# Kernel optimization log

Hardware: AMD Instinct MI355X
Metric: run time of the kernel (lower is better)

The kernel has to match this reference:

```python
import jax, jax.numpy as jnp
import numpy as np

N_NODES = 50000
N_EDGES = 800000
D_FEAT = 64          # per-node feature dim
HIDDEN = 128         # fc1 output dim; fc1 input = 2*D_FEAT


def setup_inputs() -> dict:
    key = jax.random.key(0)
    k1, k2, k3 = jax.random.split(key, 3)
    x = jax.random.normal(k1, (N_NODES, D_FEAT), dtype=jnp.float32)
    edge_index = jax.random.randint(k2, (2, N_EDGES), 0, N_NODES, dtype=jnp.int64)
    # fc1: Linear(2*D_FEAT, HIDDEN); torch Linear weight is [out, in]
    W = jax.random.normal(k3, (HIDDEN, 2 * D_FEAT), dtype=jnp.float32) * (1.0 / np.sqrt(2 * D_FEAT))
    b = jnp.zeros((HIDDEN,), dtype=jnp.float32)
    return {"x": x, "edge_index": edge_index, "W": W, "b": b}


def reference(x, edge_index, W, b):
    # Gather source-node features along edges, sum-scatter to destinations.
    src, dst = edge_index[0], edge_index[1]
    gathered = x[src]  # [E, D_FEAT] -- dominant memory traffic
    neigh = jax.ops.segment_sum(gathered, dst, num_segments=x.shape[0])  # [N, D_FEAT]
    # Concat self features with aggregated neighbor features, then Linear+ReLU.
    h = jnp.concatenate([x, neigh], axis=-1)          # [N, 2*D_FEAT]
    out = jax.nn.relu(h @ W.T + b)                    # [N, HIDDEN]
    return out
```

## Files before the change

### kernel.cpp

```cpp
#include <hip/hip_runtime.h>

#define N_NODES 50000
#define N_EDGES 800000
#define DFEAT 64
#define HID 128
#define NBKT 782
#define NSEG 196
#define SEGW 32
#define CAP 1400
#define NSTR 66

#define XB2 1563
#define WB2 8
#define EB2 196

typedef __bf16 bf16x8 __attribute__((ext_vector_type(8)));
typedef float f32x4 __attribute__((ext_vector_type(4)));

__device__ inline unsigned short f2bf(float f) {
  unsigned u = __float_as_uint(f);
  return (unsigned short)((u + 0x7FFFu + ((u >> 16) & 1u)) >> 16);
}
__device__ inline float bf2f(unsigned short h) {
  return __uint_as_float(((unsigned)h) << 16);
}

__global__ __launch_bounds__(512) void k_prep(const float* __restrict__ x,
                                              const float* __restrict__ W,
                                              const int* __restrict__ ei,
                                              unsigned short* __restrict__ xb,
                                              unsigned short* __restrict__ Wb,
                                              unsigned int* __restrict__ coarse) {
  int bid = blockIdx.x;
  const int tid = threadIdx.x;
  if (bid < XB2) {
    int t = bid * 512 + tid;
    if (t < N_NODES * DFEAT / 4) {
      float4 v = *(const float4*)&x[t * 4];
      ushort4 o = {f2bf(v.x), f2bf(v.y), f2bf(v.z), f2bf(v.w)};
      *(ushort4*)&xb[t * 4] = o;
    }
    return;
  }
  bid -= XB2;
  if (bid < WB2) {
    int t = bid * 512 + tid;
    float4 v = *(const float4*)&W[t * 4];
    ushort4 o = {f2bf(v.x), f2bf(v.y), f2bf(v.z), f2bf(v.w)};
    *(ushort4*)&Wb[t * 4] = o;
    return;
  }
  bid -= WB2;
  __shared__ int lcnt[NBKT];
  for (int i = tid; i < NBKT; i += 512) lcnt[i] = 0;
  __syncthreads();

  int e0 = (bid * 512 + tid) * 8;
  if (e0 < N_EDGES) {
    int4 sa = *(const int4*)&ei[e0];
    int4 sb = *(const int4*)&ei[e0 + 4];
    int4 da = *(const int4*)&ei[N_EDGES + e0];
    int4 db = *(const int4*)&ei[N_EDGES + e0 + 4];
    int ss[8] = {sa.x, sa.y, sa.z, sa.w, sb.x, sb.y, sb.z, sb.w};
    int dd[8] = {da.x, da.y, da.z, da.w, db.x, db.y, db.z, db.w};
#pragma unroll
    for (int i = 0; i < 8; ++i) {
      int bkt = dd[i] >> 6;
      int rank = atomicAdd(&lcnt[bkt], 1);
      if (rank < SEGW - 1)
        coarse[(size_t)bkt * (NSEG * SEGW) + bid * SEGW + 1 + rank] =
            ((unsigned)dd[i] << 16) | (unsigned)ss[i];
    }
  }
  __syncthreads();
  for (int i = tid; i < NBKT; i += 512) {
    int c = lcnt[i];
    coarse[(size_t)i * (NSEG * SEGW) + bid * SEGW] =
        (unsigned)(c < SEGW - 1 ? c : SEGW - 1);
  }
}

__global__ __launch_bounds__(512) void k_gnn(const unsigned short* __restrict__ xb,
                                             const unsigned short* __restrict__ Wb,
                                             const unsigned int* __restrict__ coarse,
                                             const float* __restrict__ bv,
                                             float* __restrict__ out) {
  __shared__ unsigned int stg[NSEG * SEGW];
  __shared__ unsigned int sq[CAP];
  __shared__ unsigned int ns_u[32 * NSTR];
  __shared__ int lcnt[64];
  __shared__ int lbase[65];

  const int tid = threadIdx.x;
  const int b = blockIdx.x;
  const int nb = b * 64;
  const unsigned int* base = coarse + (size_t)b * (NSEG * SEGW);

  if (tid < 64) lcnt[tid] = 0;
  const int NU4 = NSEG * SEGW / 4;
  for (int i = tid; i < NU4; i += 512)
    ((uint4*)stg)[i] = ((const uint4*)base)[i];
  __syncthreads();

  for (int s = tid; s < NSEG; s += 512) {
    int cs = (int)stg[s * SEGW];
    if (cs > SEGW - 1) cs = SEGW - 1;
    for (int k = 0; k < cs; ++k) {
      unsigned e = stg[s * SEGW + 1 + k] & 0x003fffffu;
      int rel = (int)(e >> 16);
      int rank = atomicAdd(&lcnt[rel], 1);
      stg[s * SEGW + 1 + k] = e | ((unsigned)rank << 22);
    }
  }
  __syncthreads();
  if (tid < 64) {
    int v = lcnt[tid];
    int inc = v;
#pragma unroll
    for (int o = 1; o < 64; o <<= 1) {
      int u = __shfl_up(inc, o);
      if (tid >= o) inc += u;
    }
    int ex = inc - v;
    lbase[tid] = ex < CAP ? ex : CAP;
    if (tid == 63) lbase[64] = inc < CAP ? inc : CAP;
  }
  __syncthreads();
  for (int s = tid; s < NSEG; s += 512) {
    int cs = (int)stg[s * SEGW];
    if (cs > SEGW - 1) cs = SEGW - 1;
    for (int k = 0; k < cs; ++k) {
      unsigned w = stg[s * SEGW + 1 + k];
      unsigned e = w & 0x003fffffu;
      int p = lbase[e >> 16] + (int)(w >> 22);
      if (p < CAP) sq[p] = e;
    }
  }
  __syncthreads();

  const int wave = tid >> 6;
  const int lane = tid & 63;
  const int g3 = lane >> 4;
  const int c = lane & 15;
  const uint2* xu2 = (const uint2*)xb;

#pragma unroll
  for (int i2 = 0; i2 < 2; ++i2) {
    int n = (wave * 4 + g3) * 2 + i2;
    int beg = lbase[n], end = lbase[n + 1];
    float A0 = 0.f, A1 = 0.f, A2 = 0.f, A3 = 0.f;
    float B0 = 0.f, B1 = 0.f, B2 = 0.f, B3 = 0.f;
    float C0 = 0.f, C1 = 0.f, C2 = 0.f, C3 = 0.f;
    float D0 = 0.f, D1 = 0.f, D2 = 0.f, D3 = 0.f;
    int j = beg;
    for (; j + 3 < end; j += 4) {
      unsigned e0 = sq[j], e1 = sq[j + 1], e2 = sq[j + 2], e3 = sq[j + 3];
      uint2 v0 = xu2[(e0 & 0xffffu) * 16 + c];
      uint2 v1 = xu2[(e1 & 0xffffu) * 16 + c];
      uint2 v2 = xu2[(e2 & 0xffffu) * 16 + c];
      uint2 v3 = xu2[(e3 & 0xffffu) * 16 + c];
      A0 += bf2f((unsigned short)(v0.x & 0xffffu)); A1 += bf2f((unsigned short)(v0.x >> 16));
      A2 += bf2f((unsigned short)(v0.y & 0xffffu)); A3 += bf2f((unsigned short)(v0.y >> 16));
      B0 += bf2f((unsigned short)(v1.x & 0xffffu)); B1 += bf2f((unsigned short)(v1.x >> 16));
      B2 += bf2f((unsigned short)(v1.y & 0xffffu)); B3 += bf2f((unsigned short)(v1.y >> 16));
      C0 += bf2f((unsigned short)(v2.x & 0xffffu)); C1 += bf2f((unsigned short)(v2.x >> 16));
      C2 += bf2f((unsigned short)(v2.y & 0xffffu)); C3 += bf2f((unsigned short)(v2.y >> 16));
      D0 += bf2f((unsigned short)(v3.x & 0xffffu)); D1 += bf2f((unsigned short)(v3.x >> 16));
      D2 += bf2f((unsigned short)(v3.y & 0xffffu)); D3 += bf2f((unsigned short)(v3.y >> 16));
    }
    for (; j < end; ++j) {
      unsigned e = sq[j];
      uint2 v = xu2[(e & 0xffffu) * 16 + c];
      A0 += bf2f((unsigned short)(v.x & 0xffffu)); A1 += bf2f((unsigned short)(v.x >> 16));
      A2 += bf2f((unsigned short)(v.y & 0xffffu)); A3 += bf2f((unsigned short)(v.y >> 16));
    }
    A0 += B0 + C0 + D0; A1 += B1 + C1 + D1;
    A2 += B2 + C2 + D2; A3 += B3 + C3 + D3;
    ns_u[(2 * c) * NSTR + n] = (unsigned)f2bf(A0) | ((unsigned)f2bf(A1) << 16);
    ns_u[(2 * c + 1) * NSTR + n] = (unsigned)f2bf(A2) | ((unsigned)f2bf(A3) << 16);
  }
  __syncthreads();

  const int g2 = wave & 3;
  const int o = wave >> 2;
  const int l15 = lane & 15;
  const int quad = lane >> 4;
  const int node0 = nb + g2 * 16;

  int anode = node0 + l15;
  if (anode >= N_NODES) anode = N_NODES - 1;
  const unsigned short* hx = xb + (size_t)anode * DFEAT;

  bf16x8 fa0 = *(const bf16x8*)(hx + quad * 8);
  bf16x8 fa1 = *(const bf16x8*)(hx + 32 + quad * 8);
  bf16x8 fa2, fa3;
  {
    int m = g2 * 16 + l15;
    union { unsigned u[4]; bf16x8 v; } c2, c3;
#pragma unroll
    for (int i = 0; i < 4; ++i) {
      c2.u[i] = ns_u[(quad * 4 + i) * NSTR + m];
      c3.u[i] = ns_u[(16 + quad * 4 + i) * NSTR + m];
    }
    fa2 = c2.v;
    fa3 = c3.v;
  }

  f32x4 accr[4];
#pragma unroll
  for (int t = 0; t < 4; ++t) accr[t] = (f32x4){0.f, 0.f, 0.f, 0.f};

#pragma unroll
  for (int t = 0; t < 4; ++t) {
    int nt = o * 4 + t;
    const unsigned short* wr = Wb + (size_t)(nt * 16 + l15) * (2 * DFEAT) + quad * 8;
    bf16x8 b0 = *(const bf16x8*)(wr);
    bf16x8 b1 = *(const bf16x8*)(wr + 32);
    bf16x8 b2 = *(const bf16x8*)(wr + 64);
    bf16x8 b3 = *(const bf16x8*)(wr + 96);
    accr[t] = __builtin_amdgcn_mfma_f32_16x16x32_bf16(fa0, b0, accr[t], 0, 0, 0);
    accr[t] = __builtin_amdgcn_mfma_f32_16x16x32_bf16(fa1, b1, accr[t], 0, 0, 0);
    accr[t] = __builtin_amdgcn_mfma_f32_16x16x32_bf16(fa2, b2, accr[t], 0, 0, 0);
    accr[t] = __builtin_amdgcn_mfma_f32_16x16x32_bf16(fa3, b3, accr[t], 0, 0, 0);
  }

#pragma unroll
  for (int t = 0; t < 4; ++t) {
    int nt = o * 4 + t;
    float bias = bv[nt * 16 + l15];
#pragma unroll
    for (int r = 0; r < 4; ++r) {
      int node = node0 + quad * 4 + r;
      if (node < N_NODES) {
        float v = accr[t][r] + bias;
        out[(size_t)node * HID + nt * 16 + l15] = v > 0.f ? v : 0.f;
      }
    }
  }
}

extern "C" void kernel_launch(void* const* d_in, const int* in_sizes, int n_in,
                              void* d_out, int out_size, void* d_ws, size_t ws_size,
                              hipStream_t stream) {
  const float* x = (const float*)d_in[0];
  const int* ei = (const int*)d_in[1];
  const float* W = (const float*)d_in[2];
  const float* b = (const float*)d_in[3];
  float* out = (float*)d_out;

  char* ws = (char*)d_ws;
  unsigned int* coarse = (unsigned int*)ws;   ws += (size_t)NBKT * NSEG * SEGW * 4;
  unsigned short* xb   = (unsigned short*)ws; ws += (size_t)N_NODES * DFEAT * 2;
  unsigned short* Wb   = (unsigned short*)ws; ws += (size_t)HID * 2 * DFEAT * 2;

  k_prep<<<XB2 + WB2 + EB2, 512, 0, stream>>>(x, W, ei, xb, Wb, coarse);
  k_gnn<<<NBKT, 512, 0, stream>>>(xb, Wb, coarse, b, out);
}
```

Baseline: 128.2 us.

## Split fused GNN into separate convert, bin, gather and FC kernels

Splits the two-kernel pipeline into four: bf16 conversion, edge binning, neighbor gather/aggregation writing bf16 sums to global memory, and an MFMA linear layer reading them back. It also pads the shared staging buffer row stride to 33 words to cut LDS bank conflicts. The split lowers per-kernel LDS use and register pressure, which may raise occupancy. The cost is two more launches and a round trip of the aggregated features through global memory.

```diff
diff --git a/kernel.cpp b/kernel.cpp
--- a/kernel.cpp
+++ b/kernel.cpp
@@ -7,8 +7,8 @@
 #define NBKT 782
 #define NSEG 196
 #define SEGW 32
+#define SSTR 33
 #define CAP 1400
-#define NSTR 66
 
 #define XB2 1563
 #define WB2 8
@@ -25,12 +25,10 @@
   return __uint_as_float(((unsigned)h) << 16);
 }
 
-__global__ __launch_bounds__(512) void k_prep(const float* __restrict__ x,
-                                              const float* __restrict__ W,
-                                              const int* __restrict__ ei,
-                                              unsigned short* __restrict__ xb,
-                                              unsigned short* __restrict__ Wb,
-                                              unsigned int* __restrict__ coarse) {
+__global__ __launch_bounds__(512) void k_cvt(const float* __restrict__ x,
+                                             const float* __restrict__ W,
+                                             unsigned short* __restrict__ xb,
+                                             unsigned short* __restrict__ Wb) {
   int bid = blockIdx.x;
   const int tid = threadIdx.x;
   if (bid < XB2) {
@@ -43,14 +41,16 @@
     return;
   }
   bid -= XB2;
-  if (bid < WB2) {
-    int t = bid * 512 + tid;
-    float4 v = *(const float4*)&W[t * 4];
-    ushort4 o = {f2bf(v.x), f2bf(v.y), f2bf(v.z), f2bf(v.w)};
-    *(ushort4*)&Wb[t * 4] = o;
-    return;
-  }
-  bid -= WB2;
+  int t = bid * 512 + tid;
+  float4 v = *(const float4*)&W[t * 4];
+  ushort4 o = {f2bf(v.x), f2bf(v.y), f2bf(v.z), f2bf(v.w)};
+  *(ushort4*)&Wb[t * 4] = o;
+}
+
+__global__ __launch_bounds__(512) void k_bin(const int* __restrict__ ei,
+                                             unsigned int* __restrict__ coarse) {
+  const int bid = blockIdx.x;
+  const int tid = threadIdx.x;
   __shared__ int lcnt[NBKT];
   for (int i = tid; i < NBKT; i += 512) lcnt[i] = 0;
   __syncthreads();
@@ -80,14 +80,12 @@
   }
 }
 
-__global__ __launch_bounds__(512) void k_gnn(const unsigned short* __restrict__ xb,
-                                             const unsigned short* __restrict__ Wb,
-                                             const unsigned int* __restrict__ coarse,
-                                             const float* __restrict__ bv,
-                                             float* __restrict__ out) {
-  __shared__ unsigned int stg[NSEG * SEGW];
+__global__ __launch_bounds__(512) void k_gather(const unsigned short* __restrict__ xb,
+                                                const unsigned int* __restrict__ coarse,
+                                                const float* __restrict__ bv,
+                                                unsigned short* __restrict__ nsg) {
+  __shared__ unsigned int stg[NSEG * SSTR];
   __shared__ unsigned int sq[CAP];
-  __shared__ unsigned int ns_u[32 * NSTR];
   __shared__ int lcnt[64];
   __shared__ int lbase[65];
 
@@ -98,18 +96,21 @@
 
   if (tid < 64) lcnt[tid] = 0;
   const int NU4 = NSEG * SEGW / 4;
-  for (int i = tid; i < NU4; i += 512)
-    ((uint4*)stg)[i] = ((const uint4*)base)[i];
+  for (int i = tid; i < NU4; i += 512) {
+    uint4 v = ((const uint4*)base)[i];
+    int s = i >> 3, w = (i & 7) * 4;
+    unsigned* p = &stg[s * SSTR + w];
+    p[0] = v.x; p[1] = v.y; p[2] = v.z; p[3] = v.w;
+  }
   __syncthreads();
 
   for (int s = tid; s < NSEG; s += 512) {
-    int cs = (int)stg[s * SEGW];
+    int cs = (int)stg[s * SSTR];
     if (cs > SEGW - 1) cs = SEGW - 1;
     for (int k = 0; k < cs; ++k) {
-      unsigned e = stg[s * SEGW + 1 + k] & 0x003fffffu;
-      int rel = (int)(e >> 16);
-      int rank = atomicAdd(&lcnt[rel], 1);
-      stg[s * SEGW + 1 + k] = e | ((unsigned)rank << 22);
+      unsigned e = stg[s * SSTR + 1 + k] & 0x003fffffu;
+      int rank = atomicAdd(&lcnt[e >> 16], 1);
+      stg[s * SSTR + 1 + k] = e | ((unsigned)rank << 22);
     }
   }
   __syncthreads();
@@ -127,10 +128,10 @@
   }
   __syncthreads();
   for (int s = tid; s < NSEG; s += 512) {
-    int cs = (int)stg[s * SEGW];
+    int cs = (int)stg[s * SSTR];
     if (cs > SEGW - 1) cs = SEGW - 1;
     for (int k = 0; k < cs; ++k) {
-      unsigned w = stg[s * SEGW + 1 + k];
+      unsigned w = stg[s * SSTR + 1 + k];
       unsigned e = w & 0x003fffffu;
       int p = lbase[e >> 16] + (int)(w >> 22);
       if (p < CAP) sq[p] = e;
@@ -176,11 +177,25 @@
     }
     A0 += B0 + C0 + D0; A1 += B1 + C1 + D1;
     A2 += B2 + C2 + D2; A3 += B3 + C3 + D3;
-    ns_u[(2 * c) * NSTR + n] = (unsigned)f2bf(A0) | ((unsigned)f2bf(A1) << 16);
-    ns_u[(2 * c + 1) * NSTR + n] = (unsigned)f2bf(A2) | ((unsigned)f2bf(A3) << 16);
-  }
-  __syncthreads();
-
+    int gn = nb + n;
+    if (gn < N_NODES) {
+      ushort4 o = {f2bf(A0), f2bf(A1), f2bf(A2), f2bf(A3)};
+      *(ushort4*)&nsg[(size_t)gn * DFEAT + 4 * c] = o;
+    }
+  }
+}
+
+__global__ __launch_bounds__(512) void k_fc(const unsigned short* __restrict__ xb,
+                                            const unsigned short* __restrict__ nsg,
+                                            const unsigned short* __restrict__ Wb,
+                                            const float* __restrict__ bv,
+                                            float* __restrict__ out) {
+  const int tid = threadIdx.x;
+  const int b = blockIdx.x;
+  const int nb = b * 64;
+
+  const int wave = tid >> 6;
+  const int lane = tid & 63;
   const int g2 = wave & 3;
   const int o = wave >> 2;
   const int l15 = lane & 15;
@@ -190,21 +205,12 @@
   int anode = node0 + l15;
   if (anode >= N_NODES) anode = N_NODES - 1;
   const unsigned short* hx = xb + (size_t)anode * DFEAT;
+  const unsigned short* hn = nsg + (size_t)anode * DFEAT;
 
   bf16x8 fa0 = *(const bf16x8*)(hx + quad * 8);
   bf16x8 fa1 = *(const bf16x8*)(hx + 32 + quad * 8);
-  bf16x8 fa2, fa3;
-  {
-    int m = g2 * 16 + l15;
-    union { unsigned u[4]; bf16x8 v; } c2, c3;
-#pragma unroll
-    for (int i = 0; i < 4; ++i) {
-      c2.u[i] = ns_u[(quad * 4 + i) * NSTR + m];
-      c3.u[i] = ns_u[(16 + quad * 4 + i) * NSTR + m];
-    }
-    fa2 = c2.v;
-    fa3 = c3.v;
-  }
+  bf16x8 fa2 = *(const bf16x8*)(hn + quad * 8);
+  bf16x8 fa3 = *(const bf16x8*)(hn + 32 + quad * 8);
 
   f32x4 accr[4];
 #pragma unroll
@@ -252,7 +258,10 @@
   unsigned int* coarse = (unsigned int*)ws;   ws += (size_t)NBKT * NSEG * SEGW * 4;
   unsigned short* xb   = (unsigned short*)ws; ws += (size_t)N_NODES * DFEAT * 2;
   unsigned short* Wb   = (unsigned short*)ws; ws += (size_t)HID * 2 * DFEAT * 2;
-
-  k_prep<<<XB2 + WB2 + EB2, 512, 0, stream>>>(x, W, ei, xb, Wb, coarse);
-  k_gnn<<<NBKT, 512, 0, stream>>>(xb, Wb, coarse, b, out);
-}
+  unsigned short* nsg  = (unsigned short*)ws; ws += (size_t)N_NODES * DFEAT * 2;
+
+  k_cvt<<<XB2 + WB2, 512, 0, stream>>>(x, W, xb, Wb);
+  k_bin<<<EB2, 512, 0, stream>>>(ei, coarse);
+  k_gather<<<NBKT, 512, 0, stream>>>(xb, coarse, b, nsg);
+  k_fc<<<NBKT, 512, 0, stream>>>(xb, nsg, Wb, b, out);
+}
```

Measured after the change: 129.7 us. Within noise of the previous version (+1.2%).

## Split bf16 features into two half tables and gather halves sequentially

Applied to the files above, without the earlier changes.

Stores the bf16 copy of x as two separate arrays holding features 0-31 and 32-63. The neighbor gather now runs in two passes, one node per 8 lanes. Each pass touches a 3.2MB table, which is meant to improve L2 hit rates for random row gathers. The staging buffer in LDS is also padded to a stride of 33 to avoid bank conflicts in the per-segment scans. In exchange, edge indices are read twice, each random access fetches only 64 bytes, and an extra barrier is added.

```diff
diff --git a/kernel.cpp b/kernel.cpp
--- a/kernel.cpp
+++ b/kernel.cpp
@@ -7,6 +7,7 @@
 #define NBKT 782
 #define NSEG 196
 #define SEGW 32
+#define SSTR 33
 #define CAP 1400
 #define NSTR 66
 
@@ -28,7 +29,8 @@
 __global__ __launch_bounds__(512) void k_prep(const float* __restrict__ x,
                                               const float* __restrict__ W,
                                               const int* __restrict__ ei,
-                                              unsigned short* __restrict__ xb,
+                                              unsigned short* __restrict__ xlo,
+                                              unsigned short* __restrict__ xhi,
                                               unsigned short* __restrict__ Wb,
                                               unsigned int* __restrict__ coarse) {
   int bid = blockIdx.x;
@@ -38,7 +40,11 @@
     if (t < N_NODES * DFEAT / 4) {
       float4 v = *(const float4*)&x[t * 4];
       ushort4 o = {f2bf(v.x), f2bf(v.y), f2bf(v.z), f2bf(v.w)};
-      *(ushort4*)&xb[t * 4] = o;
+      int node = t >> 4;
+      int f4 = (t & 15) * 4;
+      unsigned short* dst = (f4 < 32) ? &xlo[(size_t)node * 32 + f4]
+                                      : &xhi[(size_t)node * 32 + (f4 - 32)];
+      *(ushort4*)dst = o;
     }
     return;
   }
@@ -80,12 +86,49 @@
   }
 }
 
-__global__ __launch_bounds__(512) void k_gnn(const unsigned short* __restrict__ xb,
+__device__ inline void gather_half(const uint2* __restrict__ xu2,
+                                   const unsigned int* __restrict__ sq,
+                                   unsigned int* __restrict__ ns_u,
+                                   int beg, int end, int c, int n, int pb) {
+  float A0 = 0.f, A1 = 0.f, A2 = 0.f, A3 = 0.f;
+  float B0 = 0.f, B1 = 0.f, B2 = 0.f, B3 = 0.f;
+  float C0 = 0.f, C1 = 0.f, C2 = 0.f, C3 = 0.f;
+  float D0 = 0.f, D1 = 0.f, D2 = 0.f, D3 = 0.f;
+  int j = beg;
+  for (; j + 3 < end; j += 4) {
+    unsigned e0 = sq[j], e1 = sq[j + 1], e2 = sq[j + 2], e3 = sq[j + 3];
+    uint2 v0 = xu2[(e0 & 0xffffu) * 8 + c];
+    uint2 v1 = xu2[(e1 & 0xffffu) * 8 + c];
+    uint2 v2 = xu2[(e2 & 0xffffu) * 8 + c];
+    uint2 v3 = xu2[(e3 & 0xffffu) * 8 + c];
+    A0 += bf2f((unsigned short)(v0.x & 0xffffu)); A1 += bf2f((unsigned short)(v0.x >> 16));
+    A2 += bf2f((unsigned short)(v0.y & 0xffffu)); A3 += bf2f((unsigned short)(v0.y >> 16));
+    B0 += bf2f((unsigned short)(v1.x & 0xffffu)); B1 += bf2f((unsigned short)(v1.x >> 16));
+    B2 += bf2f((unsigned short)(v1.y & 0xffffu)); B3 += bf2f((unsigned short)(v1.y >> 16));
+    C0 += bf2f((unsigned short)(v2.x & 0xffffu)); C1 += bf2f((unsigned short)(v2.x >> 16));
+    C2 += bf2f((unsigned short)(v2.y & 0xffffu)); C3 += bf2f((unsigned short)(v2.y >> 16));
+    D0 += bf2f((unsigned short)(v3.x & 0xffffu)); D1 += bf2f((unsigned short)(v3.x >> 16));
+    D2 += bf2f((unsigned short)(v3.y & 0xffffu)); D3 += bf2f((unsigned short)(v3.y >> 16));
+  }
+  for (; j < end; ++j) {
+    unsigned e = sq[j];
+    uint2 v = xu2[(e & 0xffffu) * 8 + c];
+    A0 += bf2f((unsigned short)(v.x & 0xffffu)); A1 += bf2f((unsigned short)(v.x >> 16));
+    A2 += bf2f((unsigned short)(v.y & 0xffffu)); A3 += bf2f((unsigned short)(v.y >> 16));
+  }
+  A0 += B0 + C0 + D0; A1 += B1 + C1 + D1;
+  A2 += B2 + C2 + D2; A3 += B3 + C3 + D3;
+  ns_u[(pb + 2 * c) * NSTR + n]     = (unsigned)f2bf(A0) | ((unsigned)f2bf(A1) << 16);
+  ns_u[(pb + 2 * c + 1) * NSTR + n] = (unsigned)f2bf(A2) | ((unsigned)f2bf(A3) << 16);
+}
+
+__global__ __launch_bounds__(512) void k_gnn(const unsigned short* __restrict__ xlo,
+                                             const unsigned short* __restrict__ xhi,
                                              const unsigned short* __restrict__ Wb,
                                              const unsigned int* __restrict__ coarse,
                                              const float* __restrict__ bv,
                                              float* __restrict__ out) {
-  __shared__ unsigned int stg[NSEG * SEGW];
+  __shared__ unsigned int stg[NSEG * SSTR];
   __shared__ unsigned int sq[CAP];
   __shared__ unsigned int ns_u[32 * NSTR];
   __shared__ int lcnt[64];
@@ -98,18 +141,21 @@
 
   if (tid < 64) lcnt[tid] = 0;
   const int NU4 = NSEG * SEGW / 4;
-  for (int i = tid; i < NU4; i += 512)
-    ((uint4*)stg)[i] = ((const uint4*)base)[i];
+  for (int i = tid; i < NU4; i += 512) {
+    uint4 v = ((const uint4*)base)[i];
+    int s = i >> 3, w = (i & 7) * 4;
+    unsigned* p = &stg[s * SSTR + w];
+    p[0] = v.x; p[1] = v.y; p[2] = v.z; p[3] = v.w;
+  }
   __syncthreads();
 
   for (int s = tid; s < NSEG; s += 512) {
-    int cs = (int)stg[s * SEGW];
+    int cs = (int)stg[s * SSTR];
     if (cs > SEGW - 1) cs = SEGW - 1;
     for (int k = 0; k < cs; ++k) {
-      unsigned e = stg[s * SEGW + 1 + k] & 0x003fffffu;
-      int rel = (int)(e >> 16);
-      int rank = atomicAdd(&lcnt[rel], 1);
-      stg[s * SEGW + 1 + k] = e | ((unsigned)rank << 22);
+      unsigned e = stg[s * SSTR + 1 + k] & 0x003fffffu;
+      int rank = atomicAdd(&lcnt[e >> 16], 1);
+      stg[s * SSTR + 1 + k] = e | ((unsigned)rank << 22);
     }
   }
   __syncthreads();
@@ -127,10 +173,10 @@
   }
   __syncthreads();
   for (int s = tid; s < NSEG; s += 512) {
-    int cs = (int)stg[s * SEGW];
+    int cs = (int)stg[s * SSTR];
     if (cs > SEGW - 1) cs = SEGW - 1;
     for (int k = 0; k < cs; ++k) {
-      unsigned w = stg[s * SEGW + 1 + k];
+      unsigned w = stg[s * SSTR + 1 + k];
       unsigned e = w & 0x003fffffu;
       int p = lbase[e >> 16] + (int)(w >> 22);
       if (p < CAP) sq[p] = e;
@@ -140,45 +186,14 @@
 
   const int wave = tid >> 6;
   const int lane = tid & 63;
-  const int g3 = lane >> 4;
-  const int c = lane & 15;
-  const uint2* xu2 = (const uint2*)xb;
-
-#pragma unroll
-  for (int i2 = 0; i2 < 2; ++i2) {
-    int n = (wave * 4 + g3) * 2 + i2;
-    int beg = lbase[n], end = lbase[n + 1];
-    float A0 = 0.f, A1 = 0.f, A2 = 0.f, A3 = 0.f;
-    float B0 = 0.f, B1 = 0.f, B2 = 0.f, B3 = 0.f;
-    float C0 = 0.f, C1 = 0.f, C2 = 0.f, C3 = 0.f;
-    float D0 = 0.f, D1 = 0.f, D2 = 0.f, D3 = 0.f;
-    int j = beg;
-    for (; j + 3 < end; j += 4) {
-      unsigned e0 = sq[j], e1 = sq[j + 1], e2 = sq[j + 2], e3 = sq[j + 3];
-      uint2 v0 = xu2[(e0 & 0xffffu) * 16 + c];
-      uint2 v1 = xu2[(e1 & 0xffffu) * 16 + c];
-      uint2 v2 = xu2[(e2 & 0xffffu) * 16 + c];
-      uint2 v3 = xu2[(e3 & 0xffffu) * 16 + c];
-      A0 += bf2f((unsigned short)(v0.x & 0xffffu)); A1 += bf2f((unsigned short)(v0.x >> 16));
-      A2 += bf2f((unsigned short)(v0.y & 0xffffu)); A3 += bf2f((unsigned short)(v0.y >> 16));
-      B0 += bf2f((unsigned short)(v1.x & 0xffffu)); B1 += bf2f((unsigned short)(v1.x >> 16));
-      B2 += bf2f((unsigned short)(v1.y & 0xffffu)); B3 += bf2f((unsigned short)(v1.y >> 16));
-      C0 += bf2f((unsigned short)(v2.x & 0xffffu)); C1 += bf2f((unsigned short)(v2.x >> 16));
-      C2 += bf2f((unsigned short)(v2.y & 0xffffu)); C3 += bf2f((unsigned short)(v2.y >> 16));
-      D0 += bf2f((unsigned short)(v3.x & 0xffffu)); D1 += bf2f((unsigned short)(v3.x >> 16));
-      D2 += bf2f((unsigned short)(v3.y & 0xffffu)); D3 += bf2f((unsigned short)(v3.y >> 16));
-    }
-    for (; j < end; ++j) {
-      unsigned e = sq[j];
-      uint2 v = xu2[(e & 0xffffu) * 16 + c];
-      A0 += bf2f((unsigned short)(v.x & 0xffffu)); A1 += bf2f((unsigned short)(v.x >> 16));
-      A2 += bf2f((unsigned short)(v.y & 0xffffu)); A3 += bf2f((unsigned short)(v.y >> 16));
-    }
-    A0 += B0 + C0 + D0; A1 += B1 + C1 + D1;
-    A2 += B2 + C2 + D2; A3 += B3 + C3 + D3;
-    ns_u[(2 * c) * NSTR + n] = (unsigned)f2bf(A0) | ((unsigned)f2bf(A1) << 16);
-    ns_u[(2 * c + 1) * NSTR + n] = (unsigned)f2bf(A2) | ((unsigned)f2bf(A3) << 16);
-  }
+  const int g3 = lane >> 3;
+  const int c = lane & 7;
+  const int n = wave * 8 + g3;
+  const int beg = lbase[n], end = lbase[n + 1];
+
+  gather_half((const uint2*)xlo, sq, ns_u, beg, end, c, n, 0);
+  __syncthreads();
+  gather_half((const uint2*)xhi, sq, ns_u, beg, end, c, n, 16);
   __syncthreads();
 
   const int g2 = wave & 3;
@@ -189,10 +204,8 @@
 
   int anode = node0 + l15;
   if (anode >= N_NODES) anode = N_NODES - 1;
-  const unsigned short* hx = xb + (size_t)anode * DFEAT;
-
-  bf16x8 fa0 = *(const bf16x8*)(hx + quad * 8);
-  bf16x8 fa1 = *(const bf16x8*)(hx + 32 + quad * 8);
+  bf16x8 fa0 = *(const bf16x8*)(xlo + (size_t)anode * 32 + quad * 8);
+  bf16x8 fa1 = *(const bf16x8*)(xhi + (size_t)anode * 32 + quad * 8);
   bf16x8 fa2, fa3;
   {
     int m = g2 * 16 + l15;
@@ -250,9 +263,10 @@
 
   char* ws = (char*)d_ws;
   unsigned int* coarse = (unsigned int*)ws;   ws += (size_t)NBKT * NSEG * SEGW * 4;
-  unsigned short* xb   = (unsigned short*)ws; ws += (size_t)N_NODES * DFEAT * 2;
+  unsigned short* xlo  = (unsigned short*)ws; ws += (size_t)N_NODES * 32 * 2;
+  unsigned short* xhi  = (unsigned short*)ws; ws += (size_t)N_NODES * 32 * 2;
   unsigned short* Wb   = (unsigned short*)ws; ws += (size_t)HID * 2 * DFEAT * 2;
 
-  k_prep<<<XB2 + WB2 + EB2, 512, 0, stream>>>(x, W, ei, xb, Wb, coarse);
-  k_gnn<<<NBKT, 512, 0, stream>>>(xb, Wb, coarse, b, out);
-}
+  k_prep<<<XB2 + WB2 + EB2, 512, 0, stream>>>(x, W, ei, xlo, xhi, Wb, coarse);
+  k_gnn<<<NBKT, 512, 0, stream>>>(xlo, xhi, Wb, coarse, b, out);
+}
```

Result: no change. 125.9 us (-1.8%).

## Fuse prep and GNN kernels into one cooperative persistent kernel with grid sync

Applied to the files above, without the earlier changes.

Merges the binning/conversion kernel and the gather+MFMA kernel into a single cooperative launch, separated by a grid-wide barrier. Conversion blocks become grid-stride and bucket processing becomes a persistent loop over the grid. The staging buffer gets a padded stride and flattened per-edge loops instead of per-segment serial loops, and the gather unroll grows from 4 to 8 edges. This aims to remove the second launch gap and the serial per-segment work, at the cost of grid-sync overhead and fewer resident blocks per bucket pass.

```diff
diff --git a/kernel.cpp b/kernel.cpp
--- a/kernel.cpp
+++ b/kernel.cpp
@@ -1,4 +1,7 @@
 #include <hip/hip_runtime.h>
+#include <hip/hip_cooperative_groups.h>
+
+namespace cg = cooperative_groups;
 
 #define N_NODES 50000
 #define N_EDGES 800000
@@ -7,12 +10,12 @@
 #define NBKT 782
 #define NSEG 196
 #define SEGW 32
+#define SSTR 33
 #define CAP 1400
 #define NSTR 66
-
-#define XB2 1563
-#define WB2 8
-#define EB2 196
+#define GMAX 768
+#define X4 (N_NODES * DFEAT / 4)
+#define TOT4 (X4 + HID * 2 * DFEAT / 4)
 
 typedef __bf16 bf16x8 __attribute__((ext_vector_type(8)));
 typedef float f32x4 __attribute__((ext_vector_type(4)));
@@ -25,217 +28,229 @@
   return __uint_as_float(((unsigned)h) << 16);
 }
 
-__global__ __launch_bounds__(512) void k_prep(const float* __restrict__ x,
-                                              const float* __restrict__ W,
-                                              const int* __restrict__ ei,
-                                              unsigned short* __restrict__ xb,
-                                              unsigned short* __restrict__ Wb,
-                                              unsigned int* __restrict__ coarse) {
-  int bid = blockIdx.x;
-  const int tid = threadIdx.x;
-  if (bid < XB2) {
-    int t = bid * 512 + tid;
-    if (t < N_NODES * DFEAT / 4) {
-      float4 v = *(const float4*)&x[t * 4];
-      ushort4 o = {f2bf(v.x), f2bf(v.y), f2bf(v.z), f2bf(v.w)};
-      *(ushort4*)&xb[t * 4] = o;
-    }
-    return;
-  }
-  bid -= XB2;
-  if (bid < WB2) {
-    int t = bid * 512 + tid;
-    float4 v = *(const float4*)&W[t * 4];
-    ushort4 o = {f2bf(v.x), f2bf(v.y), f2bf(v.z), f2bf(v.w)};
-    *(ushort4*)&Wb[t * 4] = o;
-    return;
-  }
-  bid -= WB2;
-  __shared__ int lcnt[NBKT];
-  for (int i = tid; i < NBKT; i += 512) lcnt[i] = 0;
-  __syncthreads();
-
-  int e0 = (bid * 512 + tid) * 8;
-  if (e0 < N_EDGES) {
-    int4 sa = *(const int4*)&ei[e0];
-    int4 sb = *(const int4*)&ei[e0 + 4];
-    int4 da = *(const int4*)&ei[N_EDGES + e0];
-    int4 db = *(const int4*)&ei[N_EDGES + e0 + 4];
-    int ss[8] = {sa.x, sa.y, sa.z, sa.w, sb.x, sb.y, sb.z, sb.w};
-    int dd[8] = {da.x, da.y, da.z, da.w, db.x, db.y, db.z, db.w};
-#pragma unroll
-    for (int i = 0; i < 8; ++i) {
-      int bkt = dd[i] >> 6;
-      int rank = atomicAdd(&lcnt[bkt], 1);
-      if (rank < SEGW - 1)
-        coarse[(size_t)bkt * (NSEG * SEGW) + bid * SEGW + 1 + rank] =
-            ((unsigned)dd[i] << 16) | (unsigned)ss[i];
-    }
-  }
-  __syncthreads();
-  for (int i = tid; i < NBKT; i += 512) {
-    int c = lcnt[i];
-    coarse[(size_t)i * (NSEG * SEGW) + bid * SEGW] =
-        (unsigned)(c < SEGW - 1 ? c : SEGW - 1);
-  }
-}
-
-__global__ __launch_bounds__(512) void k_gnn(const unsigned short* __restrict__ xb,
-                                             const unsigned short* __restrict__ Wb,
-                                             const unsigned int* __restrict__ coarse,
-                                             const float* __restrict__ bv,
-                                             float* __restrict__ out) {
-  __shared__ unsigned int stg[NSEG * SEGW];
+__global__ __launch_bounds__(512, 4) void k_all(const float* __restrict__ x,
+                                                const float* __restrict__ W,
+                                                const int* __restrict__ ei,
+                                                unsigned short* __restrict__ xb,
+                                                unsigned short* __restrict__ Wb,
+                                                unsigned int* __restrict__ coarse,
+                                                const float* __restrict__ bv,
+                                                float* __restrict__ out) {
+  __shared__ unsigned int stg[NSEG * SSTR];
   __shared__ unsigned int sq[CAP];
   __shared__ unsigned int ns_u[32 * NSTR];
   __shared__ int lcnt[64];
   __shared__ int lbase[65];
 
   const int tid = threadIdx.x;
-  const int b = blockIdx.x;
-  const int nb = b * 64;
-  const unsigned int* base = coarse + (size_t)b * (NSEG * SEGW);
-
-  if (tid < 64) lcnt[tid] = 0;
-  const int NU4 = NSEG * SEGW / 4;
-  for (int i = tid; i < NU4; i += 512)
-    ((uint4*)stg)[i] = ((const uint4*)base)[i];
-  __syncthreads();
-
-  for (int s = tid; s < NSEG; s += 512) {
-    int cs = (int)stg[s * SEGW];
-    if (cs > SEGW - 1) cs = SEGW - 1;
-    for (int k = 0; k < cs; ++k) {
-      unsigned e = stg[s * SEGW + 1 + k] & 0x003fffffu;
-      int rel = (int)(e >> 16);
-      int rank = atomicAdd(&lcnt[rel], 1);
-      stg[s * SEGW + 1 + k] = e | ((unsigned)rank << 22);
+  const int bid = blockIdx.x;
+  const int grid = gridDim.x;
+
+  if (bid < NSEG) {
+    int* h = (int*)stg;
+    for (int i = tid; i < NBKT; i += 512) h[i] = 0;
+    __syncthreads();
+    int e0 = (bid * 512 + tid) * 8;
+    if (e0 < N_EDGES) {
+      int4 sa = *(const int4*)&ei[e0];
+      int4 sb = *(const int4*)&ei[e0 + 4];
+      int4 da = *(const int4*)&ei[N_EDGES + e0];
+      int4 db = *(const int4*)&ei[N_EDGES + e0 + 4];
+      int ss[8] = {sa.x, sa.y, sa.z, sa.w, sb.x, sb.y, sb.z, sb.w};
+      int dd[8] = {da.x, da.y, da.z, da.w, db.x, db.y, db.z, db.w};
+#pragma unroll
+      for (int i = 0; i < 8; ++i) {
+        int bkt = dd[i] >> 6;
+        int rank = atomicAdd(&h[bkt], 1);
+        if (rank < SEGW - 1)
+          coarse[(size_t)bkt * (NSEG * SEGW) + bid * SEGW + 1 + rank] =
+              ((unsigned)dd[i] << 16) | (unsigned)ss[i];
+      }
+    }
+    __syncthreads();
+    for (int i = tid; i < NBKT; i += 512) {
+      int c = h[i];
+      coarse[(size_t)i * (NSEG * SEGW) + bid * SEGW] =
+          (unsigned)(c < SEGW - 1 ? c : SEGW - 1);
+    }
+  } else {
+    const int ncvt = grid - NSEG;
+    for (int t = (bid - NSEG) * 512 + tid; t < TOT4; t += ncvt * 512) {
+      if (t < X4) {
+        float4 v = ((const float4*)x)[t];
+        ushort4 o = {f2bf(v.x), f2bf(v.y), f2bf(v.z), f2bf(v.w)};
+        ((ushort4*)xb)[t] = o;
+      } else {
+        float4 v = ((const float4*)W)[t - X4];
+        ushort4 o = {f2bf(v.x), f2bf(v.y), f2bf(v.z), f2bf(v.w)};
+        ((ushort4*)Wb)[t - X4] = o;
+      }
     }
   }
-  __syncthreads();
-  if (tid < 64) {
-    int v = lcnt[tid];
-    int inc = v;
-#pragma unroll
-    for (int o = 1; o < 64; o <<= 1) {
-      int u = __shfl_up(inc, o);
-      if (tid >= o) inc += u;
-    }
-    int ex = inc - v;
-    lbase[tid] = ex < CAP ? ex : CAP;
-    if (tid == 63) lbase[64] = inc < CAP ? inc : CAP;
-  }
-  __syncthreads();
-  for (int s = tid; s < NSEG; s += 512) {
-    int cs = (int)stg[s * SEGW];
-    if (cs > SEGW - 1) cs = SEGW - 1;
-    for (int k = 0; k < cs; ++k) {
-      unsigned w = stg[s * SEGW + 1 + k];
-      unsigned e = w & 0x003fffffu;
-      int p = lbase[e >> 16] + (int)(w >> 22);
-      if (p < CAP) sq[p] = e;
-    }
-  }
-  __syncthreads();
-
-  const int wave = tid >> 6;
-  const int lane = tid & 63;
-  const int g3 = lane >> 4;
-  const int c = lane & 15;
-  const uint2* xu2 = (const uint2*)xb;
-
-#pragma unroll
-  for (int i2 = 0; i2 < 2; ++i2) {
-    int n = (wave * 4 + g3) * 2 + i2;
-    int beg = lbase[n], end = lbase[n + 1];
-    float A0 = 0.f, A1 = 0.f, A2 = 0.f, A3 = 0.f;
-    float B0 = 0.f, B1 = 0.f, B2 = 0.f, B3 = 0.f;
-    float C0 = 0.f, C1 = 0.f, C2 = 0.f, C3 = 0.f;
-    float D0 = 0.f, D1 = 0.f, D2 = 0.f, D3 = 0.f;
-    int j = beg;
-    for (; j + 3 < end; j += 4) {
-      unsigned e0 = sq[j], e1 = sq[j + 1], e2 = sq[j + 2], e3 = sq[j + 3];
-      uint2 v0 = xu2[(e0 & 0xffffu) * 16 + c];
-      uint2 v1 = xu2[(e1 & 0xffffu) * 16 + c];
-      uint2 v2 = xu2[(e2 & 0xffffu) * 16 + c];
-      uint2 v3 = xu2[(e3 & 0xffffu) * 16 + c];
-      A0 += bf2f((unsigned short)(v0.x & 0xffffu)); A1 += bf2f((unsigned short)(v0.x >> 16));
-      A2 += bf2f((unsigned short)(v0.y & 0xffffu)); A3 += bf2f((unsigned short)(v0.y >> 16));
-      B0 += bf2f((unsigned short)(v1.x & 0xffffu)); B1 += bf2f((unsigned short)(v1.x >> 16));
-      B2 += bf2f((unsigned short)(v1.y & 0xffffu)); B3 += bf2f((unsigned short)(v1.y >> 16));
-      C0 += bf2f((unsigned short)(v2.x & 0xffffu)); C1 += bf2f((unsigned short)(v2.x >> 16));
-      C2 += bf2f((unsigned short)(v2.y & 0xffffu)); C3 += bf2f((unsigned short)(v2.y >> 16));
-      D0 += bf2f((unsigned short)(v3.x & 0xffffu)); D1 += bf2f((unsigned short)(v3.x >> 16));
-      D2 += bf2f((unsigned short)(v3.y & 0xffffu)); D3 += bf2f((unsigned short)(v3.y >> 16));
-    }
-    for (; j < end; ++j) {
-      unsigned e = sq[j];
-      uint2 v = xu2[(e & 0xffffu) * 16 + c];
-      A0 += bf2f((unsigned short)(v.x & 0xffffu)); A1 += bf2f((unsigned short)(v.x >> 16));
-      A2 += bf2f((unsigned short)(v.y & 0xffffu)); A3 += bf2f((unsigned short)(v.y >> 16));
-    }
-    A0 += B0 + C0 + D0; A1 += B1 + C1 + D1;
-    A2 += B2 + C2 + D2; A3 += B3 + C3 + D3;
-    ns_u[(2 * c) * NSTR + n] = (unsigned)f2bf(A0) | ((unsigned)f2bf(A1) << 16);
-    ns_u[(2 * c + 1) * NSTR + n] = (unsigned)f2bf(A2) | ((unsigned)f2bf(A3) << 16);
-  }
-  __syncthreads();
-
-  const int g2 = wave & 3;
-  const int o = wave >> 2;
-  const int l15 = lane & 15;
-  const int quad = lane >> 4;
-  const int node0 = nb + g2 * 16;
-
-  int anode = node0 + l15;
-  if (anode >= N_NODES) anode = N_NODES - 1;
-  const unsigned short* hx = xb + (size_t)anode * DFEAT;
-
-  bf16x8 fa0 = *(const bf16x8*)(hx + quad * 8);
-  bf16x8 fa1 = *(const bf16x8*)(hx + 32 + quad * 8);
-  bf16x8 fa2, fa3;
-  {
-    int m = g2 * 16 + l15;
-    union { unsigned u[4]; bf16x8 v; } c2, c3;
-#pragma unroll
-    for (int i = 0; i < 4; ++i) {
-      c2.u[i] = ns_u[(quad * 4 + i) * NSTR + m];
-      c3.u[i] = ns_u[(16 + quad * 4 + i) * NSTR + m];
-    }
-    fa2 = c2.v;
-    fa3 = c3.v;
-  }
-
-  f32x4 accr[4];
-#pragma unroll
-  for (int t = 0; t < 4; ++t) accr[t] = (f32x4){0.f, 0.f, 0.f, 0.f};
-
-#pragma unroll
-  for (int t = 0; t < 4; ++t) {
-    int nt = o * 4 + t;
-    const unsigned short* wr = Wb + (size_t)(nt * 16 + l15) * (2 * DFEAT) + quad * 8;
-    bf16x8 b0 = *(const bf16x8*)(wr);
-    bf16x8 b1 = *(const bf16x8*)(wr + 32);
-    bf16x8 b2 = *(const bf16x8*)(wr + 64);
-    bf16x8 b3 = *(const bf16x8*)(wr + 96);
-    accr[t] = __builtin_amdgcn_mfma_f32_16x16x32_bf16(fa0, b0, accr[t], 0, 0, 0);
-    accr[t] = __builtin_amdgcn_mfma_f32_16x16x32_bf16(fa1, b1, accr[t], 0, 0, 0);
-    accr[t] = __builtin_amdgcn_mfma_f32_16x16x32_bf16(fa2, b2, accr[t], 0, 0, 0);
-    accr[t] = __builtin_amdgcn_mfma_f32_16x16x32_bf16(fa3, b3, accr[t], 0, 0, 0);
-  }
-
-#pragma unroll
-  for (int t = 0; t < 4; ++t) {
-    int nt = o * 4 + t;
-    float bias = bv[nt * 16 + l15];
-#pragma unroll
-    for (int r = 0; r < 4; ++r) {
-      int node = node0 + quad * 4 + r;
-      if (node < N_NODES) {
-        float v = accr[t][r] + bias;
-        out[(size_t)node * HID + nt * 16 + l15] = v > 0.f ? v : 0.f;
-      }
-    }
+
+  cg::this_grid().sync();
+
+  for (int bk = bid; bk < NBKT; bk += grid) {
+    const unsigned int* base = coarse + (size_t)bk * (NSEG * SEGW);
+    const int nb = bk * 64;
+
+    if (tid < 64) lcnt[tid] = 0;
+    for (int i = tid; i < NSEG * SEGW / 4; i += 512) {
+      uint4 v = ((const uint4*)base)[i];
+      int s = i >> 3, w = (i & 7) * 4;
+      unsigned* p = &stg[s * SSTR + w];
+      p[0] = v.x; p[1] = v.y; p[2] = v.z; p[3] = v.w;
+    }
+    __syncthreads();
+
+    for (int i = tid; i < NSEG * (SEGW - 1); i += 512) {
+      int s = i / (SEGW - 1), k = i - s * (SEGW - 1);
+      int cs = (int)stg[s * SSTR];
+      if (k < cs) {
+        unsigned e = stg[s * SSTR + 1 + k] & 0x003fffffu;
+        int r = atomicAdd(&lcnt[e >> 16], 1);
+        stg[s * SSTR + 1 + k] = e | ((unsigned)r << 22);
+      }
+    }
+    __syncthreads();
+    if (tid < 64) {
+      int v = lcnt[tid];
+      int inc = v;
+#pragma unroll
+      for (int o = 1; o < 64; o <<= 1) {
+        int u = __shfl_up(inc, o);
+        if (tid >= o) inc += u;
+      }
+      int ex = inc - v;
+      lbase[tid] = ex < CAP ? ex : CAP;
+      if (tid == 63) lbase[64] = inc < CAP ? inc : CAP;
+    }
+    __syncthreads();
+    for (int i = tid; i < NSEG * (SEGW - 1); i += 512) {
+      int s = i / (SEGW - 1), k = i - s * (SEGW - 1);
+      int cs = (int)stg[s * SSTR];
+      if (k < cs) {
+        unsigned w2 = stg[s * SSTR + 1 + k];
+        unsigned e = w2 & 0x003fffffu;
+        int p = lbase[e >> 16] + (int)(w2 >> 22);
+        if (p < CAP) sq[p] = e;
+      }
+    }
+    __syncthreads();
+
+    const int wave = tid >> 6;
+    const int lane = tid & 63;
+    const int grp = lane >> 4;
+    const int c = lane & 15;
+    const uint2* xu2 = (const uint2*)xb;
+
+#pragma unroll
+    for (int i2 = 0; i2 < 2; ++i2) {
+      int n = (wave * 4 + grp) * 2 + i2;
+      int beg = lbase[n], end = lbase[n + 1];
+      float A0 = 0.f, A1 = 0.f, A2 = 0.f, A3 = 0.f;
+      float B0 = 0.f, B1 = 0.f, B2 = 0.f, B3 = 0.f;
+      float C0 = 0.f, C1 = 0.f, C2 = 0.f, C3 = 0.f;
+      float D0 = 0.f, D1 = 0.f, D2 = 0.f, D3 = 0.f;
+      int j = beg;
+      for (; j + 7 < end; j += 8) {
+        unsigned e0 = sq[j],     e1 = sq[j + 1], e2 = sq[j + 2], e3 = sq[j + 3];
+        unsigned e4 = sq[j + 4], e5 = sq[j + 5], e6 = sq[j + 6], e7 = sq[j + 7];
+        uint2 v0 = xu2[(e0 & 0xffffu) * 16 + c];
+        uint2 v1 = xu2[(e1 & 0xffffu) * 16 + c];
+        uint2 v2 = xu2[(e2 & 0xffffu) * 16 + c];
+        uint2 v3 = xu2[(e3 & 0xffffu) * 16 + c];
+        uint2 v4 = xu2[(e4 & 0xffffu) * 16 + c];
+        uint2 v5 = xu2[(e5 & 0xffffu) * 16 + c];
+        uint2 v6 = xu2[(e6 & 0xffffu) * 16 + c];
+        uint2 v7 = xu2[(e7 & 0xffffu) * 16 + c];
+        A0 += bf2f((unsigned short)(v0.x & 0xffffu)); A1 += bf2f((unsigned short)(v0.x >> 16));
+        A2 += bf2f((unsigned short)(v0.y & 0xffffu)); A3 += bf2f((unsigned short)(v0.y >> 16));
+        B0 += bf2f((unsigned short)(v1.x & 0xffffu)); B1 += bf2f((unsigned short)(v1.x >> 16));
+        B2 += bf2f((unsigned short)(v1.y & 0xffffu)); B3 += bf2f((unsigned short)(v1.y >> 16));
+        C0 += bf2f((unsigned short)(v2.x & 0xffffu)); C1 += bf2f((unsigned short)(v2.x >> 16));
+        C2 += bf2f((unsigned short)(v2.y & 0xffffu)); C3 += bf2f((unsigned short)(v2.y >> 16));
+        D0 += bf2f((unsigned short)(v3.x & 0xffffu)); D1 += bf2f((unsigned short)(v3.x >> 16));
+        D2 += bf2f((unsigned short)(v3.y & 0xffffu)); D3 += bf2f((unsigned short)(v3.y >> 16));
+        A0 += bf2f((unsigned short)(v4.x & 0xffffu)); A1 += bf2f((unsigned short)(v4.x >> 16));
+        A2 += bf2f((unsigned short)(v4.y & 0xffffu)); A3 += bf2f((unsigned short)(v4.y >> 16));
+        B0 += bf2f((unsigned short)(v5.x & 0xffffu)); B1 += bf2f((unsigned short)(v5.x >> 16));
+        B2 += bf2f((unsigned short)(v5.y & 0xffffu)); B3 += bf2f((unsigned short)(v5.y >> 16));
+        C0 += bf2f((unsigned short)(v6.x & 0xffffu)); C1 += bf2f((unsigned short)(v6.x >> 16));
+        C2 += bf2f((unsigned short)(v6.y & 0xffffu)); C3 += bf2f((unsigned short)(v6.y >> 16));
+        D0 += bf2f((unsigned short)(v7.x & 0xffffu)); D1 += bf2f((unsigned short)(v7.x >> 16));
+        D2 += bf2f((unsigned short)(v7.y & 0xffffu)); D3 += bf2f((unsigned short)(v7.y >> 16));
+      }
+      for (; j < end; ++j) {
+        unsigned e = sq[j];
+        uint2 v = xu2[(e & 0xffffu) * 16 + c];
+        A0 += bf2f((unsigned short)(v.x & 0xffffu)); A1 += bf2f((unsigned short)(v.x >> 16));
+        A2 += bf2f((unsigned short)(v.y & 0xffffu)); A3 += bf2f((unsigned short)(v.y >> 16));
+      }
+      A0 += B0 + C0 + D0; A1 += B1 + C1 + D1;
+      A2 += B2 + C2 + D2; A3 += B3 + C3 + D3;
+      ns_u[(2 * c) * NSTR + n]     = (unsigned)f2bf(A0) | ((unsigned)f2bf(A1) << 16);
+      ns_u[(2 * c + 1) * NSTR + n] = (unsigned)f2bf(A2) | ((unsigned)f2bf(A3) << 16);
+    }
+    __syncthreads();
+
+    const int g2 = wave & 3;
+    const int o = wave >> 2;
+    const int l15 = lane & 15;
+    const int quad = lane >> 4;
+    const int node0 = nb + g2 * 16;
+
+    int anode = node0 + l15;
+    if (anode >= N_NODES) anode = N_NODES - 1;
+    const unsigned short* hx = xb + (size_t)anode * DFEAT;
+
+    bf16x8 fa0 = *(const bf16x8*)(hx + quad * 8);
+    bf16x8 fa1 = *(const bf16x8*)(hx + 32 + quad * 8);
+    bf16x8 fa2, fa3;
+    {
+      int m = g2 * 16 + l15;
+      union { unsigned u[4]; bf16x8 v; } c2, c3;
+#pragma unroll
+      for (int i = 0; i < 4; ++i) {
+        c2.u[i] = ns_u[(quad * 4 + i) * NSTR + m];
+        c3.u[i] = ns_u[(16 + quad * 4 + i) * NSTR + m];
+      }
+      fa2 = c2.v;
+      fa3 = c3.v;
+    }
+
+    f32x4 accr[4];
+#pragma unroll
+    for (int t = 0; t < 4; ++t) accr[t] = (f32x4){0.f, 0.f, 0.f, 0.f};
+
+#pragma unroll
+    for (int t = 0; t < 4; ++t) {
+      int nt = o * 4 + t;
+      const unsigned short* wr = Wb + (size_t)(nt * 16 + l15) * (2 * DFEAT) + quad * 8;
+      bf16x8 b0 = *(const bf16x8*)(wr);
+      bf16x8 b1 = *(const bf16x8*)(wr + 32);
+      bf16x8 b2 = *(const bf16x8*)(wr + 64);
+      bf16x8 b3 = *(const bf16x8*)(wr + 96);
+      accr[t] = __builtin_amdgcn_mfma_f32_16x16x32_bf16(fa0, b0, accr[t], 0, 0, 0);
+      accr[t] = __builtin_amdgcn_mfma_f32_16x16x32_bf16(fa1, b1, accr[t], 0, 0, 0);
+      accr[t] = __builtin_amdgcn_mfma_f32_16x16x32_bf16(fa2, b2, accr[t], 0, 0, 0);
+      accr[t] = __builtin_amdgcn_mfma_f32_16x16x32_bf16(fa3, b3, accr[t], 0, 0, 0);
+    }
+
+#pragma unroll
+    for (int t = 0; t < 4; ++t) {
+      int nt = o * 4 + t;
+      float bias = bv[nt * 16 + l15];
+#pragma unroll
+      for (int r = 0; r < 4; ++r) {
+        int node = node0 + quad * 4 + r;
+        if (node < N_NODES) {
+          float v = accr[t][r] + bias;
+          out[(size_t)node * HID + nt * 16 + l15] = v > 0.f ? v : 0.f;
+        }
+      }
+    }
+    __syncthreads();
   }
 }
 
@@ -253,6 +268,18 @@
   unsigned short* xb   = (unsigned short*)ws; ws += (size_t)N_NODES * DFEAT * 2;
   unsigned short* Wb   = (unsigned short*)ws; ws += (size_t)HID * 2 * DFEAT * 2;
 
-  k_prep<<<XB2 + WB2 + EB2, 512, 0, stream>>>(x, W, ei, xb, Wb, coarse);
-  k_gnn<<<NBKT, 512, 0, stream>>>(xb, Wb, coarse, b, out);
-}
+  static int grid = 0;
+  if (grid == 0) {
+    int occ = 0;
+    hipOccupancyMaxActiveBlocksPerMultiprocessor(&occ, (const void*)k_all, 512, 0);
+    if (occ < 1) occ = 1;
+    grid = occ * 256;
+    if (grid > GMAX) grid = GMAX;
+    if (grid <= NSEG) grid = NSEG + 60;
+  }
+
+  void* args[] = {(void*)&x, (void*)&W, (void*)&ei, (void*)&xb,
+                  (void*)&Wb, (void*)&coarse, (void*)&b, (void*)&out};
+  hipLaunchCooperativeKernel((const void*)k_all, dim3(grid), dim3(512),
+                             args, 0, stream);
+}
```

Measured after the change: 207.5 us. 61.9% more time.
